# Performance work log

Measured on AMD Instinct MI355X. Metric: run time of the kernel, lower is better.

Reference implementation:

```python
import jax, jax.numpy as jnp
import numpy as np

EPS = 1e-8


def setup_inputs() -> dict:
    key = jax.random.key(0)
    ks = jax.random.split(key, 5)
    n = 256
    K, K2, Q = 8, 8, 2
    J = 10                      # scales * Q
    F = K * J + 1               # first-layer filters + low-pass
    F2 = 5 * K2 + 1             # second-layer filters + low-pass
    return {
        "x_hat": jax.random.normal(ks[0], (n, n, 2), dtype=jnp.float32),
        "psi_hat_real": jax.random.normal(ks[1], (F, n, n), dtype=jnp.float32),
        "psi_hat_imag": jax.random.normal(ks[2], (F, n, n), dtype=jnp.float32),
        "psi_hat_real2": jax.random.normal(ks[3], (F2, n, n), dtype=jnp.float32),
        "psi_hat_imag2": jax.random.normal(ks[4], (F2, n, n), dtype=jnp.float32),
        "K": K,
        "K2": K2,
        "Q": Q,
    }


def _forward(x_hat, psi_hat_real, psi_hat_imag, psi_hat_real2, psi_hat_imag2, K, K2, Q):
    n = psi_hat_real.shape[1]
    psi = psi_hat_real + 1j * psi_hat_imag                    # [F,n,n] complex
    psi2 = psi_hat_real2 ** 2 + psi_hat_imag2 ** 2            # [F2,n,n] real
    xc = x_hat[..., 0] + 1j * x_hat[..., 1]                   # [n,n]

    # first-layer wavelet transform: ifft2 of freq-domain product, then modulus
    conv = jnp.fft.ifft2(xc[None] * psi)                      # [F,n,n]
    mod = jnp.sqrt(conv.real ** 2 + conv.imag ** 2 + EPS)     # [F,n,n]

    a = mod[-1]                                               # low-pass channel
    a_hat = jnp.fft.fft2(a)                                   # [n,n] complex
    J = (psi.shape[0] - 1) // K
    p = mod[:-1].reshape(K, J, n, n)
    P = jnp.fft.fft2(p)                                       # [K,J,n,n] complex

    norm = 1.0 / (n * n)
    psi2c = psi2.astype(P.dtype)

    # s0: |mean(|a_hat|^2 * psi2[-1])|
    s0 = jnp.sqrt(jnp.mean(jnp.abs(a_hat) ** 2 * psi2[-1]) ** 2 + EPS)[None]

    # same-scale cross spectra: M[f,i1,i2,j] = mean_xy(P[i1,j] conj(P[i2,j]) psi2[f])
    cross_same = P[:, None] * jnp.conj(P[None])               # [K,K,J,n,n]
    M = jnp.einsum('abjxy,fxy->fabj', cross_same, psi2c) * norm
    Mmag = jnp.sqrt(M.real ** 2 + M.imag ** 2 + EPS)          # [F2,K,K,J]

    # cross-scale, same orientation: N[f,i,j,l] = mean_xy(P[i,j] conj(P[i,l]) psi2[f])
    cross_jl = P[:, :, None] * jnp.conj(P[:, None, :])        # [K,J,J,n,n]
    N = jnp.einsum('ijlxy,fxy->fijl', cross_jl, psi2c) * norm
    Nmag = jnp.sqrt(N.real ** 2 + N.imag ** 2 + EPS)          # [F2,K,J,J]

    # covariance with low-pass: A[f,i,j] = mean_xy(P[i,j] conj(a_hat) psi2[4*K2+f])
    crossA = P * jnp.conj(a_hat)                              # [K,J,n,n]
    A = jnp.einsum('ijxy,fxy->fij', crossA, psi2c[4 * K2:]) * norm
    Amag = jnp.sqrt(A.real ** 2 + A.imag ** 2 + EPS)          # [K2+1,K,J]

    # assemble output in the exact order of the original nested loops
    parts = [s0]
    for j in range(J):
        fs = min(j // Q, 4) * K2
        for i in range(K):
            parts.append(Mmag[fs:, i, i:, j].reshape(-1))     # [(F2-fs)*(K-i)]
            for l in range(j + 1, J):
                fs2 = min(l // 2, 4) * K2                     # original hardcodes //2
                parts.append(Nmag[fs2:, i, j, l])
            parts.append(Amag[:, i, j])
    return jnp.concatenate(parts)


def reference(x_hat, psi_hat_real, psi_hat_imag, psi_hat_real2, psi_hat_imag2, K, K2, Q):
    return _forward(x_hat, psi_hat_real, psi_hat_imag, psi_hat_real2, psi_hat_imag2, K, K2, Q)
```

## Files before the change

### kernel.cpp

```cpp
#include <hip/hip_runtime.h>
#include <math.h>

#define NN 256
#define NPIX 65536
#define NFIELD 81
#define NF2 41
#define FPAD 48
#define NPAIR_PAD 1024
#define KC 16
#define CSTR 257
#define NSPL 128
#define KPB (NPIX / NSPL)
#define NCHK (KPB / KC)
#define EPSF 1e-8f


__device__ inline void make_tw(float* twc, float* tws, int tid, int nthr) {
    for (int i = tid; i < 128; i += nthr) {
        float ang = (float)i * (6.283185307179586f / 256.0f);
        twc[i] = cosf(ang);
        tws[i] = sinf(ang);
    }
}

template<int T>
__device__ inline void dif_fft(float2* row, const float* twc, const float* tws,
                               float sgn, int lane) {
    #pragma unroll
    for (int s = 0; s < 8; ++s) {
        int half = 128 >> s;
        __syncthreads();
        #pragma unroll
        for (int bi = 0; bi < 128 / T; ++bi) {
            int b = lane + bi * T;
            int t = b & (half - 1);
            int blk = b >> (7 - s);
            int p0 = (blk << (8 - s)) + t;
            float2 u = row[p0];
            float2 v = row[p0 + half];
            row[p0] = make_float2(u.x + v.x, u.y + v.y);
            float dx = u.x - v.x, dy = u.y - v.y;
            int w = t << s;
            float c = twc[w], si = sgn * tws[w];
            row[p0 + half] = make_float2(dx * c - dy * si, dx * si + dy * c);
        }
    }
    __syncthreads();
}

template<int T>
__device__ inline void dit_fft(float2* row, const float* twc, const float* tws,
                               float sgn, int lane) {
    #pragma unroll
    for (int s = 0; s < 8; ++s) {
        int half = 1 << s;
        __syncthreads();
        #pragma unroll
        for (int bi = 0; bi < 128 / T; ++bi) {
            int b = lane + bi * T;
            int t = b & (half - 1);
            int blk = b >> s;
            int p0 = (blk << (s + 1)) + t;
            int w = t << (7 - s);
            float c = twc[w], si = sgn * tws[w];
            float2 v = row[p0 + half];
            float vx = v.x * c - v.y * si;
            float vy = v.x * si + v.y * c;
            float2 u = row[p0];
            row[p0] = make_float2(u.x + vx, u.y + vy);
            row[p0 + half] = make_float2(u.x - vx, u.y - vy);
        }
    }
    __syncthreads();
}

__global__ void k0_psit(const float* __restrict__ r, const float* __restrict__ im,
                        float* __restrict__ psit) {
    __shared__ float tile[64 * FPAD];
    int tid = threadIdx.x;
    int base = blockIdx.x * 64;
    for (int idx = tid; idx < NF2 * 64; idx += 256) {
        int f = idx >> 6, px = idx & 63;
        size_t g = (size_t)f * NPIX + base + px;
        float a = r[g], b = im[g];
        tile[px * FPAD + f] = a * a + b * b;
    }
    for (int idx = tid; idx < 64 * (FPAD - NF2); idx += 256) {
        int px = idx / (FPAD - NF2), f = NF2 + idx % (FPAD - NF2);
        tile[px * FPAD + f] = 0.f;
    }
    __syncthreads();
    for (int idx = tid; idx < 64 * FPAD; idx += 256)
        psit[(size_t)base * FPAD + idx] = tile[idx];
}

__global__ void k1_rowifft(const float* __restrict__ xhat,
                           const float* __restrict__ psiR,
                           const float* __restrict__ psiI,
                           float2* __restrict__ P) {
    __shared__ float2 buf[4][257];
    __shared__ float twc[128], tws[128];
    int tid = threadIdx.x;
    make_tw(twc, tws, tid, 256);
    int fi = tid >> 6, lane = tid & 63;
    int f = blockIdx.y;
    int y = blockIdx.x * 4 + fi;
    const float inv = 1.0f / 256.0f;
    size_t rb = (size_t)f * NPIX + (size_t)y * NN;
    for (int j = lane; j < NN; j += 64) {
        float xr = xhat[(y * NN + j) * 2 + 0];
        float xi = xhat[(y * NN + j) * 2 + 1];
        float pr = psiR[rb + j], pi = psiI[rb + j];
        buf[fi][j] = make_float2((xr * pr - xi * pi) * inv, (xr * pi + xi * pr) * inv);
    }
    dif_fft<64>(&buf[fi][0], twc, tws, +1.0f, lane);
    for (int j = lane; j < NN; j += 64) P[rb + j] = buf[fi][j];
}

__global__ void k2_colpass(float2* __restrict__ P) {
    __shared__ float2 buf[16][257];
    __shared__ float twc[128], tws[128];
    int tid = threadIdx.x;
    make_tw(twc, tws, tid, 256);
    int c = tid & 15, tl = tid >> 4;
    int f = blockIdx.y;
    int xb = blockIdx.x * 16;
    size_t fb = (size_t)f * NPIX;
    #pragma unroll
    for (int i = 0; i < 16; ++i) {
        int y = tl + i * 16;
        buf[c][y] = P[fb + (size_t)y * NN + xb + c];
    }
    dif_fft<16>(&buf[c][0], twc, tws, +1.0f, tl);
    const float inv = 1.0f / 256.0f;
    #pragma unroll
    for (int i = 0; i < 16; ++i) {
        int p = tl + i * 16;
        float2 v = buf[c][p];
        float vx = v.x * inv, vy = v.y * inv;
        buf[c][p] = make_float2(sqrtf(vx * vx + vy * vy + EPSF), 0.0f);
    }
    dit_fft<16>(&buf[c][0], twc, tws, -1.0f, tl);
    #pragma unroll
    for (int i = 0; i < 16; ++i) {
        int y = tl + i * 16;
        P[fb + (size_t)y * NN + xb + c] = buf[c][y];
    }
}

__global__ void k3_rowfft(float2* __restrict__ P) {
    __shared__ float2 buf[4][257];
    __shared__ float twc[128], tws[128];
    int tid = threadIdx.x;
    make_tw(twc, tws, tid, 256);
    int fi = tid >> 6, lane = tid & 63;
    int f = blockIdx.y;
    int y = blockIdx.x * 4 + fi;
    size_t rb = (size_t)f * NPIX + (size_t)y * NN;
    for (int j = lane; j < NN; j += 64) buf[fi][j] = P[rb + j];
    dit_fft<64>(&buf[fi][0], twc, tws, -1.0f, lane);
    for (int j = lane; j < NN; j += 64) P[rb + j] = buf[fi][j];
}

__device__ __host__ inline int fsj(int j) { int t = j >> 1; return (t > 4 ? 4 : t) * 8; }

__device__ inline int group_of(int s) {
    return (s < 80) ? 0 : (s < 192) ? 1 : (s < 336) ? 2 : (s < 512) ? 3 : 4;
}

__device__ inline void pair_sorted(int s, int& u, int& v) {
    if (s >= 800) { u = 80; v = 80; return; }
    const int Gs[5] = {0, 80, 192, 336, 512};
    int g = group_of(s);
    int r = s - Gs[g];
    if (r < 72) {
        int j = 2 * g + (r >= 36);
        int rr = (r >= 36) ? r - 36 : r;
        int a = 0;
        while (rr >= 8 - a) { rr -= 8 - a; ++a; }
        int b = a + rr;
        u = a * 10 + j; v = b * 10 + j;
        return;
    }
    int r2 = r - 72;
    int l0 = 2 * g;
    int c0 = (l0 >= 1) ? 8 * l0 : 0;
    if (r2 < c0) { int i = r2 / l0, j = r2 % l0; u = i * 10 + j; v = i * 10 + l0; return; }
    r2 -= c0;
    int l1 = 2 * g + 1;
    if (r2 < 8 * l1) { int i = r2 / l1, j = r2 % l1; u = i * 10 + j; v = i * 10 + l1; return; }
    r2 -= 8 * l1;
    u = r2; v = 80;
}

__device__ inline int pM(int a, int b, int j) {
    const int Gt[5] = {0, 80, 192, 336, 512};
    return Gt[j >> 1] + (j & 1) * 36 + a * 8 - a * (a - 1) / 2 + (b - a);
}
__device__ inline int pN(int i, int j, int l) {
    const int Gt[5] = {0, 80, 192, 336, 512};
    return Gt[l >> 1] + 72 + ((l & 1) ? 8 * (l - 1) : 0) + i * l + j;
}

__global__ void __launch_bounds__(256) c1all(const float2* __restrict__ P,
                                             const float* __restrict__ psit,
                                             float* __restrict__ Mpart) {
    __shared__ float2 Cl[KC * CSTR];
    __shared__ float  psl[KC * 16];
    __shared__ int    su[256], sv[256];
    int tid = threadIdx.x;
    int split = blockIdx.x, y = blockIdx.y;
    int z    = (y == 0) ? 0 : (y <= 2) ? 1 : 2;
    int tile = (y == 0) ? 0 : (y <= 2) ? (y - 1) : (y - 3);
    int pbase = tile * 256;
    {
        int u, v;
        pair_sorted(pbase + tid, u, v);
        su[tid] = u; sv[tid] = v;
    }
    int lane = tid & 63;
    int wv = tid >> 6;
    int qp = wv >> 1;
    int half = wv & 1;
    int p0 = half * 128 + lane;
    int kl = tid & 15, prow = tid >> 4;
    float ar[2][4][2], ai[2][4][2];
    #pragma unroll
    for (int a = 0; a < 2; ++a)
        #pragma unroll
        for (int b = 0; b < 4; ++b)
            #pragma unroll
            for (int c = 0; c < 2; ++c) { ar[a][b][c] = 0.f; ai[a][b][c] = 0.f; }

    for (int ch = 0; ch < NCHK; ++ch) {
        int kb = split * KPB + ch * KC;
        __syncthreads();
        psl[tid] = psit[(size_t)(kb + (tid >> 4)) * FPAD + z * 16 + (tid & 15)];
        #pragma unroll 4
        for (int i = 0; i < 16; ++i) {
            int pair = prow + 16 * i;
            int u = su[pair], v = sv[pair];
            float2 A = P[(size_t)u * NPIX + kb + kl];
            float2 B = P[(size_t)v * NPIX + kb + kl];
            Cl[kl * CSTR + pair] = make_float2(A.x * B.x + A.y * B.y,
                                               A.y * B.x - A.x * B.y);
        }
        __syncthreads();
        #pragma unroll 4
        for (int k = 0; k < KC; ++k) {
            float4 pA = *(const float4*)&psl[k * 16 + qp * 8];
            float4 pB = *(const float4*)&psl[k * 16 + qp * 8 + 4];
            float2 cc0 = Cl[k * CSTR + p0];
            float2 cc1 = Cl[k * CSTR + p0 + 64];
            float pq[2][4] = {{pA.x, pA.y, pA.z, pA.w}, {pB.x, pB.y, pB.z, pB.w}};
            float cr[2] = {cc0.x, cc1.x};
            float ci[2] = {cc0.y, cc1.y};
            #pragma unroll
            for (int qq = 0; qq < 2; ++qq)
                #pragma unroll
                for (int fi = 0; fi < 4; ++fi)
                    #pragma unroll
                    for (int m = 0; m < 2; ++m) {
                        ar[qq][fi][m] += pq[qq][fi] * cr[m];
                        ai[qq][fi][m] += pq[qq][fi] * ci[m];
                    }
        }
    }
    float2* out = (float2*)Mpart + (size_t)(y * NSPL + split) * 4096;
    #pragma unroll
    for (int qq = 0; qq < 2; ++qq)
        #pragma unroll
        for (int fi = 0; fi < 4; ++fi)
            #pragma unroll
            for (int m = 0; m < 2; ++m) {
                int fl = (qp * 2 + qq) * 4 + fi;
                out[fl * 256 + p0 + m * 64] = make_float2(ar[qq][fi][m], ai[qq][fi][m]);
            }
}

__global__ void __launch_bounds__(256) c1red(const float* __restrict__ Mpart,
                                             float* __restrict__ Mout) {
    int y = blockIdx.x, fl = blockIdx.y;
    int pl = threadIdx.x;
    int z    = (y == 0) ? 0 : (y <= 2) ? 1 : 2;
    int tile = (y == 0) ? 0 : (y <= 2) ? (y - 1) : (y - 3);
    const float2* mp = (const float2*)Mpart;
    size_t cell = (size_t)fl * 256 + pl;
    float sx = 0.f, sy = 0.f;
    #pragma unroll 8
    for (int sp = 0; sp < NSPL; ++sp) {
        float2 v = mp[(size_t)(y * NSPL + sp) * 4096 + cell];
        sx += v.x; sy += v.y;
    }
    int f = z * 16 + fl, p = tile * 256 + pl;
    ((float2*)Mout)[(size_t)f * NPAIR_PAD + p] = make_float2(sx, sy);
}

__device__ inline int seglen_d(int j, int i) {
    int s = (NF2 - fsj(j)) * (8 - i) + 9;
    for (int l = j + 1; l < 10; ++l) s += NF2 - fsj(l);
    return s;
}

__device__ inline float magof(const float* Mout, int f, int p) {
    const float nrm = 1.0f / 65536.0f;
    float re = Mout[((size_t)f * NPAIR_PAD + p) * 2 + 0] * nrm;
    float im = Mout[((size_t)f * NPAIR_PAD + p) * 2 + 1] * nrm;
    return sqrtf(re * re + im * im + EPSF);
}

__global__ void c2_assemble(const float* __restrict__ Mout, float* __restrict__ out) {
    int bid = blockIdx.x, tid = threadIdx.x;
    if (bid == 0) {
        if (tid == 0) out[0] = magof(Mout, 40, 800);
        return;
    }
    int idx = bid - 1;
    int j = idx / 8, i = idx % 8;
    int base = 1;
    for (int q = 0; q < idx; ++q) base += seglen_d(q / 8, q % 8);
    int fs = fsj(j);
    int d = 8 - i;
    int len1 = (NF2 - fs) * d;
    int total = seglen_d(j, i);
    for (int e = tid; e < total; e += 256) {
        int f, p;
        if (e < len1) {
            f = fs + e / d;
            int b = i + e % d;
            p = pM(i, b, j);
        } else {
            int e2 = e - len1;
            bool found = false;
            f = 0; p = 0;
            for (int l = j + 1; l < 10; ++l) {
                int ll = NF2 - fsj(l);
                if (e2 < ll) {
                    f = fsj(l) + e2;
                    p = pN(i, j, l);
                    found = true;
                    break;
                }
                e2 -= ll;
            }
            if (!found) { f = 32 + e2; p = 720 + i * 10 + j; }
        }
        out[base + e] = magof(Mout, f, p);
    }
}

extern "C" void kernel_launch(void* const* d_in, const int* in_sizes, int n_in,
                              void* d_out, int out_size, void* d_ws, size_t ws_size,
                              hipStream_t stream) {
    const float* xhat  = (const float*)d_in[0];
    const float* psiR  = (const float*)d_in[1];
    const float* psiI  = (const float*)d_in[2];
    const float* p2R   = (const float*)d_in[3];
    const float* p2I   = (const float*)d_in[4];

    char* ws = (char*)d_ws;
    float2* P = (float2*)ws;
    size_t off = (size_t)NFIELD * NPIX * sizeof(float2);
    float* psit = (float*)(ws + off);
    off += (size_t)NPIX * FPAD * sizeof(float);
    float* Mpart = (float*)(ws + off);
    off += (size_t)7 * NSPL * 4096 * 2 * sizeof(float);
    float* Mout = (float*)(ws + off);

    k0_psit<<<dim3(NPIX / 64), dim3(256), 0, stream>>>(p2R, p2I, psit);
    k1_rowifft<<<dim3(64, NFIELD), dim3(256), 0, stream>>>(xhat, psiR, psiI, P);
    k2_colpass<<<dim3(16, NFIELD), dim3(256), 0, stream>>>(P);
    k3_rowfft<<<dim3(64, NFIELD), dim3(256), 0, stream>>>(P);
    c1all<<<dim3(NSPL, 7), dim3(256), 0, stream>>>(P, psit, Mpart);
    c1red<<<dim3(7, 16), dim3(256), 0, stream>>>(Mpart, Mout);
    c2_assemble<<<dim3(81), dim3(256), 0, stream>>>(Mout, (float*)d_out);
}
```

Measured before the change: 407.7 us.

## Double-buffer cross-spectrum staging in c1all with register-prefetched loads

Restructures the c1all main loop into a two-stage software pipeline: global loads of P and psi for the next chunk are issued into registers before the FMA loop over the current chunk, then written into the alternate shared buffer afterwards. This hides global memory latency behind compute and cuts the barriers per chunk from two to one. The pair index lookups move from shared memory into precomputed per-thread register offsets. To fit two buffers, the chunk size KC is halved, which doubles the number of iterations and raises register pressure, possibly lowering occupancy.

```diff
diff --git a/kernel.cpp b/kernel.cpp
--- a/kernel.cpp
+++ b/kernel.cpp
@@ -7,7 +7,7 @@
 #define NF2 41
 #define FPAD 48
 #define NPAIR_PAD 1024
-#define KC 16
+#define KC 8
 #define CSTR 257
 #define NSPL 128
 #define KPB (NPIX / NSPL)
@@ -205,25 +205,33 @@
 __global__ void __launch_bounds__(256) c1all(const float2* __restrict__ P,
                                              const float* __restrict__ psit,
                                              float* __restrict__ Mpart) {
-    __shared__ float2 Cl[KC * CSTR];
-    __shared__ float  psl[KC * 16];
-    __shared__ int    su[256], sv[256];
+    __shared__ float2 Cl[2][KC][CSTR];
+    __shared__ float  psl[2][KC][16];
     int tid = threadIdx.x;
     int split = blockIdx.x, y = blockIdx.y;
     int z    = (y == 0) ? 0 : (y <= 2) ? 1 : 2;
     int tile = (y == 0) ? 0 : (y <= 2) ? (y - 1) : (y - 3);
     int pbase = tile * 256;
-    {
+
+    int kl = tid & 7;
+    int prow = tid >> 3;
+    int uoff[8], voff[8];
+    #pragma unroll
+    for (int i = 0; i < 8; ++i) {
         int u, v;
-        pair_sorted(pbase + tid, u, v);
-        su[tid] = u; sv[tid] = v;
-    }
+        pair_sorted(pbase + prow + 32 * i, u, v);
+        uoff[i] = u * NPIX;
+        voff[i] = v * NPIX;
+    }
+    int pk = tid >> 4, pf = tid & 15;
+    bool do_psi = tid < 128;
+
     int lane = tid & 63;
     int wv = tid >> 6;
     int qp = wv >> 1;
     int half = wv & 1;
     int p0 = half * 128 + lane;
-    int kl = tid & 15, prow = tid >> 4;
+
     float ar[2][4][2], ai[2][4][2];
     #pragma unroll
     for (int a = 0; a < 2; ++a)
@@ -232,26 +240,41 @@
             #pragma unroll
             for (int c = 0; c < 2; ++c) { ar[a][b][c] = 0.f; ai[a][b][c] = 0.f; }
 
+    float2 Ast[8], Bst[8];
+    float psv = 0.f;
+
+    auto issue = [&](int ch) {
+        int kb = split * KPB + ch * KC;
+        #pragma unroll
+        for (int i = 0; i < 8; ++i) {
+            Ast[i] = P[(size_t)(uoff[i] + kb + kl)];
+            Bst[i] = P[(size_t)(voff[i] + kb + kl)];
+        }
+        if (do_psi) psv = psit[(size_t)(kb + pk) * FPAD + z * 16 + pf];
+    };
+    auto write_staged = [&](int buf) {
+        #pragma unroll
+        for (int i = 0; i < 8; ++i) {
+            Cl[buf][kl][prow + 32 * i] = make_float2(
+                Ast[i].x * Bst[i].x + Ast[i].y * Bst[i].y,
+                Ast[i].y * Bst[i].x - Ast[i].x * Bst[i].y);
+        }
+        if (do_psi) psl[buf][pk][pf] = psv;
+    };
+
+    issue(0);
+    write_staged(0);
+    __syncthreads();
+
     for (int ch = 0; ch < NCHK; ++ch) {
-        int kb = split * KPB + ch * KC;
-        __syncthreads();
-        psl[tid] = psit[(size_t)(kb + (tid >> 4)) * FPAD + z * 16 + (tid & 15)];
-        #pragma unroll 4
-        for (int i = 0; i < 16; ++i) {
-            int pair = prow + 16 * i;
-            int u = su[pair], v = sv[pair];
-            float2 A = P[(size_t)u * NPIX + kb + kl];
-            float2 B = P[(size_t)v * NPIX + kb + kl];
-            Cl[kl * CSTR + pair] = make_float2(A.x * B.x + A.y * B.y,
-                                               A.y * B.x - A.x * B.y);
-        }
-        __syncthreads();
-        #pragma unroll 4
+        int cur = ch & 1;
+        if (ch + 1 < NCHK) issue(ch + 1);
+        #pragma unroll
         for (int k = 0; k < KC; ++k) {
-            float4 pA = *(const float4*)&psl[k * 16 + qp * 8];
-            float4 pB = *(const float4*)&psl[k * 16 + qp * 8 + 4];
-            float2 cc0 = Cl[k * CSTR + p0];
-            float2 cc1 = Cl[k * CSTR + p0 + 64];
+            float4 pA = *(const float4*)&psl[cur][k][qp * 8];
+            float4 pB = *(const float4*)&psl[cur][k][qp * 8 + 4];
+            float2 cc0 = Cl[cur][k][p0];
+            float2 cc1 = Cl[cur][k][p0 + 64];
             float pq[2][4] = {{pA.x, pA.y, pA.z, pA.w}, {pB.x, pB.y, pB.z, pB.w}};
             float cr[2] = {cc0.x, cc1.x};
             float ci[2] = {cc0.y, cc1.y};
@@ -265,7 +288,10 @@
                         ai[qq][fi][m] += pq[qq][fi] * ci[m];
                     }
         }
-    }
+        if (ch + 1 < NCHK) write_staged(cur ^ 1);
+        __syncthreads();
+    }
+
     float2* out = (float2*)Mpart + (size_t)(y * NSPL + split) * 4096;
     #pragma unroll
     for (int qq = 0; qq < 2; ++qq)
```

New measurement: 401.4 us. About the same (-1.5%).
